# Optimization experiments

Measured on AMD Instinct MI355X. Metric: run time of the kernel, lower is better.

The kernel has to match this reference:

```python
import jax, jax.numpy as jnp
import numpy as np

B, S, D = 4, 2048, 1024
H = 16
HD = D // H


def setup_inputs() -> dict:
    key = jax.random.key(0)
    ks = jax.random.split(key, 5)
    scale = 0.02
    return {
        "x": jax.random.normal(ks[0], (B, S, D), dtype=jnp.float32),
        "wq": jax.random.normal(ks[1], (D, D), dtype=jnp.float32) * scale,
        "wk": jax.random.normal(ks[2], (D, D), dtype=jnp.float32) * scale,
        "wv": jax.random.normal(ks[3], (D, D), dtype=jnp.float32) * scale,
        "wo": jax.random.normal(ks[4], (D, D), dtype=jnp.float32) * scale,
    }


def reference(x, wq, wk, wv, wo):
    b, s, _ = x.shape
    # project and split heads: [b, h, s, hd]
    def proj(w):
        return jnp.einsum('bsd,de->bse', x, w).reshape(b, s, H, HD).transpose(0, 2, 1, 3)
    q, k, v = proj(wq), proj(wk), proj(wv)
    scores = jnp.einsum('bhqd,bhkd->bhqk', q, k)
    causal = jnp.tril(jnp.ones((s, s), dtype=bool))  # True = keep
    scores = jnp.where(causal, scores, -jnp.inf)
    attn = jax.nn.softmax(scores / jnp.sqrt(jnp.float32(HD)), axis=-1)
    ctx = jnp.einsum('bhqk,bhkd->bhqd', attn, v)
    ctx = ctx.transpose(0, 2, 1, 3).reshape(b, s, D)
    return jnp.einsum('bsd,de->bse', ctx, wo)
```

## Files before the change

### kernel.cpp

```cpp
#include <hip/hip_runtime.h>

#define S_LEN 2048
#define D_DIM 1024
#define NH    16
#define HD    64
#define BATCH 4
#define M_ROWS 8192

typedef __attribute__((ext_vector_type(8))) short bf16x8;
typedef __attribute__((ext_vector_type(4))) float f32x4;
typedef __attribute__((ext_vector_type(16))) float f32x16;
typedef __attribute__((ext_vector_type(8))) unsigned short u16x8;

__device__ __forceinline__ unsigned short f2bf(float f) {
    unsigned u = __builtin_bit_cast(unsigned, f);
    u = (u + 0x7fffu + ((u >> 16) & 1u)) >> 16;
    return (unsigned short)u;
}

__device__ __forceinline__ void gload16(const void* g, void* l) {
    __builtin_amdgcn_global_load_lds((const __attribute__((address_space(1))) unsigned*)g,
                                     (__attribute__((address_space(3))) unsigned*)l,
                                     16, 0, 0);
}

template<int N> __device__ __forceinline__ void vmwait() {
    if constexpr (N == 0)      asm volatile("s_waitcnt vmcnt(0)" ::: "memory");
    else if constexpr (N == 3) asm volatile("s_waitcnt vmcnt(3)" ::: "memory");
    else if constexpr (N == 5) asm volatile("s_waitcnt vmcnt(5)" ::: "memory");
}

__device__ __forceinline__ unsigned cvtpk_bf16(float lo, float hi) {
    unsigned r;
    asm("v_cvt_pk_bf16_f32 %0, %1, %2" : "=v"(r) : "v"(lo), "v"(hi));
    return r;
}
__device__ __forceinline__ void pl32swap(unsigned &a, unsigned &b) {
    asm("v_permlane32_swap_b32 %0, %1" : "+v"(a), "+v"(b));
}

__global__ __launch_bounds__(256) void prep_k(const float* __restrict__ x,
                                              const float* __restrict__ w0, const float* __restrict__ w1,
                                              const float* __restrict__ w2, const float* __restrict__ w3,
                                              unsigned short* __restrict__ xbf,
                                              unsigned short* __restrict__ o0, unsigned short* __restrict__ o1,
                                              unsigned short* __restrict__ o2, unsigned short* __restrict__ o3) {
    __shared__ float sT[64][65];
    const int t = threadIdx.x;
    if (blockIdx.x < 4096) {
        size_t i = (size_t)blockIdx.x * 256 + t;
        const float4* xf = (const float4*)x;
        float4 a = xf[2 * i], b = xf[2 * i + 1];
        u16x8 v;
        v[0] = f2bf(a.x); v[1] = f2bf(a.y); v[2] = f2bf(a.z); v[3] = f2bf(a.w);
        v[4] = f2bf(b.x); v[5] = f2bf(b.y); v[6] = f2bf(b.z); v[7] = f2bf(b.w);
        *(u16x8*)(xbf + i * 8) = v;
        return;
    }
    const int wb = blockIdx.x - 4096;
    const int z = wb >> 8;
    const float* w; unsigned short* o;
    switch (z) {
        case 0: w = w0; o = o0; break;
        case 1: w = w1; o = o1; break;
        case 2: w = w2; o = o2; break;
        default: w = w3; o = o3; break;
    }
    const float sc = (z == 0) ? 0.18033688011112042f : 1.0f;
    const int n0 = (wb & 15) * 64, k0 = ((wb >> 4) & 15) * 64;
    const int r = t >> 4, cq = t & 15;
#pragma unroll
    for (int it = 0; it < 4; ++it) {
        int k = r + it * 16;
        float4 v = *(const float4*)&w[(size_t)(k0 + k) * D_DIM + n0 + cq * 4];
        sT[k][cq * 4 + 0] = v.x; sT[k][cq * 4 + 1] = v.y;
        sT[k][cq * 4 + 2] = v.z; sT[k][cq * 4 + 3] = v.w;
    }
    __syncthreads();
    const int n = t >> 2, ch = t & 3;
    union { unsigned short s[8]; uint4 v; } p0, p1;
#pragma unroll
    for (int j = 0; j < 8; ++j) p0.s[j] = f2bf(sT[ch * 16 + j][n] * sc);
#pragma unroll
    for (int j = 0; j < 8; ++j) p1.s[j] = f2bf(sT[ch * 16 + 8 + j][n] * sc);
    *(uint4*)&o[(size_t)(n0 + n) * D_DIM + k0 + ch * 16]     = p0.v;
    *(uint4*)&o[(size_t)(n0 + n) * D_DIM + k0 + ch * 16 + 8] = p1.v;
}

template<int MFRAG, int NFRAG, int AGLD, int BGLD>
__device__ __forceinline__ void gemm_core(const unsigned short* __restrict__ A,
                                          const unsigned short* __restrict__ Bt,
                                          unsigned short* __restrict__ sA,
                                          unsigned short* __restrict__ sB,
                                          int m0, int n0, int t,
                                          f32x4 (&acc)[MFRAG][NFRAG])
{
    constexpr int NGLD  = AGLD + BGLD;
    constexpr int ASLOT = AGLD * 4096;
    constexpr int BSLOT = BGLD * 4096;
    constexpr int NPH   = MFRAG / 2;

    const int lane = t & 63, wid = t >> 6;
    const int mm = lane & 15, quad = lane >> 4;
    const int wm = wid >> 2, wn = wid & 3;

    const int sr = t >> 2;
    const int sg = (t & 3) ^ ((sr >> 1) & 3);
    const unsigned short* asrc = A  + (size_t)(m0 + sr) * D_DIM + sg * 8;
    const unsigned short* bsrc = Bt + (size_t)(n0 + sr) * D_DIM + sg * 8;
    unsigned short* dA = sA + t * 8;
    unsigned short* dB = sB + t * 8;

    const int al = wm * (MFRAG * 16) + mm;
    const int bl = wn * (NFRAG * 16) + mm;
    const int xs = quad ^ ((mm >> 1) & 3);

#pragma unroll
    for (int pt = 0; pt < 2; ++pt) {
        const int ko = pt * 32;
#pragma unroll
        for (int i = 0; i < AGLD; ++i)
            gload16(asrc + (size_t)i * 128 * D_DIM + ko, dA + pt * ASLOT + i * 4096);
#pragma unroll
        for (int i = 0; i < BGLD; ++i)
            gload16(bsrc + (size_t)i * 128 * D_DIM + ko, dB + pt * BSLOT + i * 4096);
    }
    vmwait<NGLD>();
    __builtin_amdgcn_s_barrier();

    int sRead = 0, sWrite = 2;
    for (int T = 0; T < 32; ++T) {
        const int soA = sRead * ASLOT, soB = sRead * BSLOT;
        const int woA = sWrite * ASLOT, woB = sWrite * BSLOT;
        const int ko = (T + 2) * 32;
        const bool st = (T <= 29);

        bf16x8 bv[NFRAG];
#pragma unroll
        for (int p = 0; p < NPH; ++p) {
            if (p == 0) {
#pragma unroll
                for (int nf = 0; nf < NFRAG; ++nf)
                    bv[nf] = *(const bf16x8*)&sB[soB + (bl + nf * 16) * 32 + xs * 8];
            }
            bf16x8 af0 = *(const bf16x8*)&sA[soA + (al + (2 * p) * 16) * 32 + xs * 8];
            bf16x8 af1 = *(const bf16x8*)&sA[soA + (al + (2 * p + 1) * 16) * 32 + xs * 8];

            if (st) {
                if (p == 0) {
#pragma unroll
                    for (int i = 0; i < AGLD; ++i)
                        gload16(asrc + (size_t)i * 128 * D_DIM + ko, dA + woA + i * 4096);
                } else {
#pragma unroll
                    for (int i = 0; i < BGLD; ++i)
                        if ((i % (NPH - 1)) == p - 1)
                            gload16(bsrc + (size_t)i * 128 * D_DIM + ko, dB + woB + i * 4096);
                }
            }

            __builtin_amdgcn_s_barrier();
            asm volatile("s_waitcnt lgkmcnt(0)" ::: "memory");
            __builtin_amdgcn_s_setprio(1);
#pragma unroll
            for (int nf = 0; nf < NFRAG; ++nf) {
                acc[2 * p][nf]     = __builtin_amdgcn_mfma_f32_16x16x32_bf16(af0, bv[nf], acc[2 * p][nf], 0, 0, 0);
                acc[2 * p + 1][nf] = __builtin_amdgcn_mfma_f32_16x16x32_bf16(af1, bv[nf], acc[2 * p + 1][nf], 0, 0, 0);
            }
            __builtin_amdgcn_s_setprio(0);
            if (p == NPH - 1) {
                if (T <= 29)      vmwait<NGLD>();
                else if (T == 30) vmwait<0>();
            }
            __builtin_amdgcn_s_barrier();
        }

        sRead  = (sRead  == 2) ? 0 : sRead + 1;
        sWrite = (sWrite == 2) ? 0 : sWrite + 1;
    }
}

__global__ __launch_bounds__(512, 2) void gemmqkv_k(const unsigned short* __restrict__ A,
                                                    const unsigned short* __restrict__ Bt,
                                                    unsigned short* __restrict__ qb,
                                                    unsigned short* __restrict__ kb,
                                                    unsigned short* __restrict__ vt)
{
    __shared__ unsigned short sA[3 * 2 * 4096];
    __shared__ unsigned short sB[3 * 3 * 4096];
    const int t = threadIdx.x;
    const int bid = blockIdx.x;
    const int wg = (bid & 7) * 32 + (bid >> 3);
    const int mt = wg >> 3, nt = wg & 7;
    const int m0 = mt * 256, n0 = nt * 384;

    f32x4 acc[8][6];
#pragma unroll
    for (int i = 0; i < 8; ++i)
#pragma unroll
        for (int j = 0; j < 6; ++j) acc[i][j] = (f32x4){0.f, 0.f, 0.f, 0.f};

    gemm_core<8, 6, 2, 3>(A, Bt, sA, sB, m0, n0, t, acc);

    const int lane = t & 63, wid = t >> 6;
    const int mm = lane & 15, quad = lane >> 4;
    const int wm = wid >> 2, wn = wid & 3;

#pragma unroll
    for (int nf = 0; nf < 6; ++nf) {
        const int c0 = n0 + wn * 96 + nf * 16;
        const int widx = c0 >> 10, nl0 = c0 & 1023;
        if (widx == 2) {
            const int h = nl0 >> 6, hd = (nl0 & 63) + mm;
#pragma unroll
            for (int mf = 0; mf < 8; ++mf) {
                int rglob = m0 + wm * 128 + mf * 16 + quad * 4;
                int bb = rglob >> 11, ss = rglob & (S_LEN - 1);
                union { unsigned short s[4]; unsigned long long ll; } pk;
#pragma unroll
                for (int r = 0; r < 4; ++r) pk.s[r] = f2bf(acc[mf][nf][r]);
                *(unsigned long long*)&vt[((size_t)(bb * NH + h) * HD + hd) * S_LEN + ss] = pk.ll;
            }
        } else {
            unsigned short* outp = widx ? kb : qb;
#pragma unroll
            for (int mf = 0; mf < 8; ++mf)
#pragma unroll
                for (int r = 0; r < 4; ++r)
                    outp[(size_t)(m0 + wm * 128 + mf * 16 + quad * 4 + r) * D_DIM +
                         nl0 + mm] = f2bf(acc[mf][nf][r]);
        }
    }
}

__global__ __launch_bounds__(512, 2) void gemmo_k(const unsigned short* __restrict__ A,
                                                  const unsigned short* __restrict__ Bt,
                                                  float* __restrict__ C)
{
    __shared__ unsigned short sA[3 * 4096];
    __shared__ unsigned short sB[3 * 2 * 4096];
    const int t = threadIdx.x;
    const int bid = blockIdx.x;
    const int wg = (bid & 7) * 32 + (bid >> 3);
    const int mt = wg >> 2, nt = wg & 3;
    const int m0 = mt * 128, n0 = nt * 256;

    f32x4 acc[4][4];
#pragma unroll
    for (int i = 0; i < 4; ++i)
#pragma unroll
        for (int j = 0; j < 4; ++j) acc[i][j] = (f32x4){0.f, 0.f, 0.f, 0.f};

    gemm_core<4, 4, 1, 2>(A, Bt, sA, sB, m0, n0, t, acc);

    const int lane = t & 63, wid = t >> 6;
    const int mm = lane & 15, quad = lane >> 4;
    const int wm = wid >> 2, wn = wid & 3;

#pragma unroll
    for (int mf = 0; mf < 4; ++mf)
#pragma unroll
        for (int nf = 0; nf < 4; ++nf)
#pragma unroll
            for (int r = 0; r < 4; ++r)
                C[(size_t)(m0 + wm * 64 + mf * 16 + quad * 4 + r) * D_DIM +
                  n0 + wn * 64 + nf * 16 + mm] = acc[mf][nf][r];
}

__global__ __launch_bounds__(256, 4) void attn_k(const unsigned short* __restrict__ Q,
                                                 const unsigned short* __restrict__ K,
                                                 const unsigned short* __restrict__ Vt,
                                                 unsigned short* __restrict__ ctx)
{
    __shared__ unsigned short sK [2][64 * 64];
    __shared__ unsigned short sVT[2][64 * 64];
    const int t = threadIdx.x;
    const int lane = t & 63, w = t >> 6;
    const int m5 = lane & 31, h = lane >> 5;
    const int m7 = m5 & 7;
    const int bid = blockIdx.x;
    const int c = bid & 255, j = bid >> 8;
    const int xcd = c & 7, u = (c >> 3) & 3, bhl = c >> 5;
    const int bh = xcd * 8 + bhl;
    const int qt = 4 * j + ((j & 1) ? (3 - u) : u);
    const int b = bh >> 4, hh = bh & 15;
    const size_t rowbase = (size_t)b * S_LEN;
    const int coff = hh * HD;
    const unsigned short* Vh = Vt + (size_t)bh * HD * S_LEN;

    const int sc = t >> 3, sj = t & 7;
    const int sg = (sj ^ (sc & 7)) * 8;

    u16x8 onesu;
#pragma unroll
    for (int jj = 0; jj < 8; ++jj) onesu[jj] = 0x3F80;
    const bf16x8 ones = __builtin_bit_cast(bf16x8, onesu);

    const int q0 = qt * 128;
    const int qrw = q0 + w * 32;
    const int qr  = qrw + m5;

    bf16x8 qf[4];
#pragma unroll
    for (int s = 0; s < 4; ++s)
        qf[s] = *(const bf16x8*)(Q + (rowbase + qr) * D_DIM + coff + s * 16 + h * 8);

    f32x16 o0, o1, l16;
#pragma unroll
    for (int r = 0; r < 16; ++r) { o0[r] = 0.f; o1[r] = 0.f; l16[r] = 0.f; }

    const int nkt = 2 * qt + 2;

    gload16(K  + (rowbase + sc) * D_DIM + coff + sg,      (void*)&sK[0][t * 8]);
    gload16(K  + (rowbase + sc + 32) * D_DIM + coff + sg, (void*)&sK[0][2048 + t * 8]);
    gload16(Vh + (size_t)sc * S_LEN + sg,                 (void*)&sVT[0][t * 8]);
    gload16(Vh + (size_t)(sc + 32) * S_LEN + sg,          (void*)&sVT[0][2048 + t * 8]);

    for (int kt = 0; kt < nkt; ++kt) {
        const int buf = kt & 1;
        __syncthreads();
        if (kt + 1 < nkt) {
            const int k1 = (kt + 1) * 64;
            gload16(K  + (rowbase + k1 + sc) * D_DIM + coff + sg,      (void*)&sK[1 - buf][t * 8]);
            gload16(K  + (rowbase + k1 + sc + 32) * D_DIM + coff + sg, (void*)&sK[1 - buf][2048 + t * 8]);
            gload16(Vh + (size_t)sc * S_LEN + k1 + sg,                 (void*)&sVT[1 - buf][t * 8]);
            gload16(Vh + (size_t)(sc + 32) * S_LEN + k1 + sg,          (void*)&sVT[1 - buf][2048 + t * 8]);
        }
        const int k0 = kt * 64;
        if (k0 > qrw + 31) continue;

        f32x16 s0, s1;
#pragma unroll
        for (int r = 0; r < 16; ++r) { s0[r] = 0.f; s1[r] = 0.f; }
        __builtin_amdgcn_s_setprio(1);
#pragma unroll
        for (int s = 0; s < 4; ++s) {
            const int sl = ((2 * s + h) ^ m7) * 8;
            bf16x8 ak0 = *(const bf16x8*)&sK[buf][m5 * 64 + sl];
            bf16x8 ak1 = *(const bf16x8*)&sK[buf][(32 + m5) * 64 + sl];
            s0 = __builtin_amdgcn_mfma_f32_32x32x16_bf16(ak0, qf[s], s0, 0, 0, 0);
            s1 = __builtin_amdgcn_mfma_f32_32x32x16_bf16(ak1, qf[s], s1, 0, 0, 0);
        }
        __builtin_amdgcn_s_setprio(0);

        const bool needmask = (k0 + 63) > qrw;
        bf16x8 pb[4];
#pragma unroll
        for (int kf = 0; kf < 2; ++kf) {
            unsigned pw[8];
#pragma unroll
            for (int jj = 0; jj < 8; ++jj) {
                float plo = __builtin_amdgcn_exp2f(kf ? s1[2 * jj] : s0[2 * jj]);
                float phi = __builtin_amdgcn_exp2f(kf ? s1[2 * jj + 1] : s0[2 * jj + 1]);
                if (needmask) {
                    const int kb_ = k0 + kf * 32 + 4 * h;
                    const int r0 = 2 * jj, r1 = 2 * jj + 1;
                    if (kb_ + (r0 & 3) + 8 * (r0 >> 2) > qr) plo = 0.f;
                    if (kb_ + (r1 & 3) + 8 * (r1 >> 2) > qr) phi = 0.f;
                }
                pw[jj] = cvtpk_bf16(plo, phi);
            }
            pl32swap(pw[0], pw[2]);
            pl32swap(pw[1], pw[3]);
            pl32swap(pw[4], pw[6]);
            pl32swap(pw[5], pw[7]);
            union { unsigned u4[4]; bf16x8 v; } f0, f1;
            f0.u4[0] = pw[0]; f0.u4[1] = pw[1]; f0.u4[2] = pw[2]; f0.u4[3] = pw[3];
            f1.u4[0] = pw[4]; f1.u4[1] = pw[5]; f1.u4[2] = pw[6]; f1.u4[3] = pw[7];
            pb[kf * 2 + 0] = f0.v;
            pb[kf * 2 + 1] = f1.v;
        }

        __builtin_amdgcn_s_setprio(1);
#pragma unroll
        for (int s = 0; s < 4; ++s) {
            const int sl = ((2 * s + h) ^ m7) * 8;
            bf16x8 vf0 = *(const bf16x8*)&sVT[buf][m5 * 64 + sl];
            bf16x8 vf1 = *(const bf16x8*)&sVT[buf][(32 + m5) * 64 + sl];
            l16 = __builtin_amdgcn_mfma_f32_32x32x16_bf16(ones, pb[s], l16, 0, 0, 0);
            o0  = __builtin_amdgcn_mfma_f32_32x32x16_bf16(vf0,  pb[s], o0, 0, 0, 0);
            o1  = __builtin_amdgcn_mfma_f32_32x32x16_bf16(vf1,  pb[s], o1, 0, 0, 0);
        }
        __builtin_amdgcn_s_setprio(0);
    }

    const float linv = 1.f / l16[0];
#pragma unroll
    for (int hf = 0; hf < 2; ++hf) {
#pragma unroll
        for (int rg = 0; rg < 4; ++rg) {
            union { unsigned short s4[4]; unsigned long long ll; } pk4;
#pragma unroll
            for (int r = 0; r < 4; ++r)
                pk4.s4[r] = f2bf((hf ? o1[rg * 4 + r] : o0[rg * 4 + r]) * linv);
            *(unsigned long long*)&ctx[(rowbase + qr) * D_DIM + coff + hf * 32 + 8 * rg + 4 * h] = pk4.ll;
        }
    }
}

extern "C" void kernel_launch(void* const* d_in, const int* in_sizes, int n_in,
                              void* d_out, int out_size, void* d_ws, size_t ws_size,
                              hipStream_t stream)
{
    const float* x  = (const float*)d_in[0];
    const float* wq = (const float*)d_in[1];
    const float* wk = (const float*)d_in[2];
    const float* wv = (const float*)d_in[3];
    const float* wo = (const float*)d_in[4];

    const size_t XE = (size_t)M_ROWS * D_DIM;
    const size_t WE = (size_t)D_DIM * D_DIM;
    unsigned short* ws  = (unsigned short*)d_ws;
    unsigned short* xbf = ws;
    unsigned short* wt0 = xbf + XE;
    unsigned short* wt1 = wt0 + WE;
    unsigned short* wt2 = wt1 + WE;
    unsigned short* wt3 = wt2 + WE;
    unsigned short* qb  = wt3 + WE;
    unsigned short* kb  = qb + XE;
    unsigned short* vt  = kb + XE;
    unsigned short* cb  = vt + XE;

    prep_k<<<dim3(4096 + 1024), 256, 0, stream>>>(x, wq, wk, wv, wo,
                                                  xbf, wt0, wt1, wt2, wt3);

    gemmqkv_k<<<dim3(256), 512, 0, stream>>>(xbf, wt0, qb, kb, vt);

    attn_k<<<dim3(1024), 256, 0, stream>>>(qb, kb, vt, cb);

    gemmo_k<<<dim3(256), 512, 0, stream>>>(cb, wt3, (float*)d_out);
}
```

Measured before the change: 238.4 us.

## Split causal attention KV ranges into balanced halves with separate combine kernel

Each attention block now processes two half-workloads: strip a's first KV range and strip (15-a)'s second KV range, so every block does roughly equal causal work. Unnormalized partial outputs and row sums are written in fp32 to a workspace, and a new combine kernel sums the two partials per strip, normalizes, and converts to bf16 ctx. This targets the load imbalance of the causal triangle across blocks. In exchange it adds about 64 MB of fp32 partial traffic and an extra kernel launch, and it relies on the workspace being large enough.

```diff
diff --git a/kernel.cpp b/kernel.cpp
--- a/kernel.cpp
+++ b/kernel.cpp
@@ -270,7 +270,8 @@
 __global__ __launch_bounds__(256, 4) void attn_k(const unsigned short* __restrict__ Q,
                                                  const unsigned short* __restrict__ K,
                                                  const unsigned short* __restrict__ Vt,
-                                                 unsigned short* __restrict__ ctx)
+                                                 float* __restrict__ PO,
+                                                 float* __restrict__ PL)
 {
     __shared__ unsigned short sK [2][64 * 64];
     __shared__ unsigned short sVT[2][64 * 64];
@@ -279,10 +280,8 @@
     const int m5 = lane & 31, h = lane >> 5;
     const int m7 = m5 & 7;
     const int bid = blockIdx.x;
-    const int c = bid & 255, j = bid >> 8;
-    const int xcd = c & 7, u = (c >> 3) & 3, bhl = c >> 5;
+    const int xcd = bid & 7, bhl = (bid >> 3) & 7, a = bid >> 6;
     const int bh = xcd * 8 + bhl;
-    const int qt = 4 * j + ((j & 1) ? (3 - u) : u);
     const int b = bh >> 4, hh = bh & 15;
     const size_t rowbase = (size_t)b * S_LEN;
     const int coff = hh * HD;
@@ -296,105 +295,145 @@
     for (int jj = 0; jj < 8; ++jj) onesu[jj] = 0x3F80;
     const bf16x8 ones = __builtin_bit_cast(bf16x8, onesu);
 
-    const int q0 = qt * 128;
-    const int qrw = q0 + w * 32;
-    const int qr  = qrw + m5;
-
-    bf16x8 qf[4];
-#pragma unroll
-    for (int s = 0; s < 4; ++s)
-        qf[s] = *(const bf16x8*)(Q + (rowbase + qr) * D_DIM + coff + s * 16 + h * 8);
-
-    f32x16 o0, o1, l16;
-#pragma unroll
-    for (int r = 0; r < 16; ++r) { o0[r] = 0.f; o1[r] = 0.f; l16[r] = 0.f; }
-
-    const int nkt = 2 * qt + 2;
-
-    gload16(K  + (rowbase + sc) * D_DIM + coff + sg,      (void*)&sK[0][t * 8]);
-    gload16(K  + (rowbase + sc + 32) * D_DIM + coff + sg, (void*)&sK[0][2048 + t * 8]);
-    gload16(Vh + (size_t)sc * S_LEN + sg,                 (void*)&sVT[0][t * 8]);
-    gload16(Vh + (size_t)(sc + 32) * S_LEN + sg,          (void*)&sVT[0][2048 + t * 8]);
-
-    for (int kt = 0; kt < nkt; ++kt) {
-        const int buf = kt & 1;
+#pragma unroll 1
+    for (int jidx = 0; jidx < 2; ++jidx) {
+        const int strip = jidx ? (15 - a) : a;
+        const int ktlo  = jidx ? (strip + 1) : 0;
+        const int kthi  = jidx ? (2 * strip + 1) : strip;
+
+        const int q0 = strip * 128;
+        const int qrw = q0 + w * 32;
+        const int qr  = qrw + m5;
+
+        bf16x8 qf[4];
+#pragma unroll
+        for (int s = 0; s < 4; ++s)
+            qf[s] = *(const bf16x8*)(Q + (rowbase + qr) * D_DIM + coff + s * 16 + h * 8);
+
+        f32x16 o0, o1, l16;
+#pragma unroll
+        for (int r = 0; r < 16; ++r) { o0[r] = 0.f; o1[r] = 0.f; l16[r] = 0.f; }
+
+        {
+            const int k1 = ktlo * 64;
+            gload16(K  + (rowbase + k1 + sc) * D_DIM + coff + sg,      (void*)&sK[0][t * 8]);
+            gload16(K  + (rowbase + k1 + sc + 32) * D_DIM + coff + sg, (void*)&sK[0][2048 + t * 8]);
+            gload16(Vh + (size_t)sc * S_LEN + k1 + sg,                 (void*)&sVT[0][t * 8]);
+            gload16(Vh + (size_t)(sc + 32) * S_LEN + k1 + sg,          (void*)&sVT[0][2048 + t * 8]);
+        }
+
+        for (int kt = ktlo; kt <= kthi; ++kt) {
+            const int buf = (kt - ktlo) & 1;
+            __syncthreads();
+            if (kt < kthi) {
+                const int k1 = (kt + 1) * 64;
+                gload16(K  + (rowbase + k1 + sc) * D_DIM + coff + sg,      (void*)&sK[1 - buf][t * 8]);
+                gload16(K  + (rowbase + k1 + sc + 32) * D_DIM + coff + sg, (void*)&sK[1 - buf][2048 + t * 8]);
+                gload16(Vh + (size_t)sc * S_LEN + k1 + sg,                 (void*)&sVT[1 - buf][t * 8]);
+                gload16(Vh + (size_t)(sc + 32) * S_LEN + k1 + sg,          (void*)&sVT[1 - buf][2048 + t * 8]);
+            }
+            const int k0 = kt * 64;
+            if (k0 > qrw + 31) continue;
+
+            f32x16 s0, s1;
+#pragma unroll
+            for (int r = 0; r < 16; ++r) { s0[r] = 0.f; s1[r] = 0.f; }
+            __builtin_amdgcn_s_setprio(1);
+#pragma unroll
+            for (int s = 0; s < 4; ++s) {
+                const int sl = ((2 * s + h) ^ m7) * 8;
+                bf16x8 ak0 = *(const bf16x8*)&sK[buf][m5 * 64 + sl];
+                bf16x8 ak1 = *(const bf16x8*)&sK[buf][(32 + m5) * 64 + sl];
+                s0 = __builtin_amdgcn_mfma_f32_32x32x16_bf16(ak0, qf[s], s0, 0, 0, 0);
+                s1 = __builtin_amdgcn_mfma_f32_32x32x16_bf16(ak1, qf[s], s1, 0, 0, 0);
+            }
+            __builtin_amdgcn_s_setprio(0);
+
+            const bool needmask = (k0 + 63) > qrw;
+            bf16x8 pb[4];
+#pragma unroll
+            for (int kf = 0; kf < 2; ++kf) {
+                unsigned pw[8];
+#pragma unroll
+                for (int jj = 0; jj < 8; ++jj) {
+                    float plo = __builtin_amdgcn_exp2f(kf ? s1[2 * jj] : s0[2 * jj]);
+                    float phi = __builtin_amdgcn_exp2f(kf ? s1[2 * jj + 1] : s0[2 * jj + 1]);
+                    if (needmask) {
+                        const int kb_ = k0 + kf * 32 + 4 * h;
+                        const int r0 = 2 * jj, r1 = 2 * jj + 1;
+                        if (kb_ + (r0 & 3) + 8 * (r0 >> 2) > qr) plo = 0.f;
+                        if (kb_ + (r1 & 3) + 8 * (r1 >> 2) > qr) phi = 0.f;
+                    }
+                    pw[jj] = cvtpk_bf16(plo, phi);
+                }
+                pl32swap(pw[0], pw[2]);
+                pl32swap(pw[1], pw[3]);
+                pl32swap(pw[4], pw[6]);
+                pl32swap(pw[5], pw[7]);
+                union { unsigned u4[4]; bf16x8 v; } f0, f1;
+                f0.u4[0] = pw[0]; f0.u4[1] = pw[1]; f0.u4[2] = pw[2]; f0.u4[3] = pw[3];
+                f1.u4[0] = pw[4]; f1.u4[1] = pw[5]; f1.u4[2] = pw[6]; f1.u4[3] = pw[7];
+                pb[kf * 2 + 0] = f0.v;
+                pb[kf * 2 + 1] = f1.v;
+            }
+
+            __builtin_amdgcn_s_setprio(1);
+#pragma unroll
+            for (int s = 0; s < 4; ++s) {
+                const int sl = ((2 * s + h) ^ m7) * 8;
+                bf16x8 vf0 = *(const bf16x8*)&sVT[buf][m5 * 64 + sl];
+                bf16x8 vf1 = *(const bf16x8*)&sVT[buf][(32 + m5) * 64 + sl];
+                l16 = __builtin_amdgcn_mfma_f32_32x32x16_bf16(ones, pb[s], l16, 0, 0, 0);
+                o0  = __builtin_amdgcn_mfma_f32_32x32x16_bf16(vf0,  pb[s], o0, 0, 0, 0);
+                o1  = __builtin_amdgcn_mfma_f32_32x32x16_bf16(vf1,  pb[s], o1, 0, 0, 0);
+            }
+            __builtin_amdgcn_s_setprio(0);
+        }
         __syncthreads();
-        if (kt + 1 < nkt) {
-            const int k1 = (kt + 1) * 64;
-            gload16(K  + (rowbase + k1 + sc) * D_DIM + coff + sg,      (void*)&sK[1 - buf][t * 8]);
-            gload16(K  + (rowbase + k1 + sc + 32) * D_DIM + coff + sg, (void*)&sK[1 - buf][2048 + t * 8]);
-            gload16(Vh + (size_t)sc * S_LEN + k1 + sg,                 (void*)&sVT[1 - buf][t * 8]);
-            gload16(Vh + (size_t)(sc + 32) * S_LEN + k1 + sg,          (void*)&sVT[1 - buf][2048 + t * 8]);
+
+        const int jid = ((bh << 4) + strip) * 2 + jidx;
+        float* po = PO + (size_t)jid * 8192;
+        const int ql = w * 32 + m5;
+#pragma unroll
+        for (int hf = 0; hf < 2; ++hf) {
+#pragma unroll
+            for (int rg = 0; rg < 4; ++rg) {
+                f32x4 v;
+#pragma unroll
+                for (int r = 0; r < 4; ++r) v[r] = hf ? o1[rg * 4 + r] : o0[rg * 4 + r];
+                *(f32x4*)&po[ql * 64 + hf * 32 + 8 * rg + 4 * h] = v;
+            }
         }
-        const int k0 = kt * 64;
-        if (k0 > qrw + 31) continue;
-
-        f32x16 s0, s1;
-#pragma unroll
-        for (int r = 0; r < 16; ++r) { s0[r] = 0.f; s1[r] = 0.f; }
-        __builtin_amdgcn_s_setprio(1);
-#pragma unroll
-        for (int s = 0; s < 4; ++s) {
-            const int sl = ((2 * s + h) ^ m7) * 8;
-            bf16x8 ak0 = *(const bf16x8*)&sK[buf][m5 * 64 + sl];
-            bf16x8 ak1 = *(const bf16x8*)&sK[buf][(32 + m5) * 64 + sl];
-            s0 = __builtin_amdgcn_mfma_f32_32x32x16_bf16(ak0, qf[s], s0, 0, 0, 0);
-            s1 = __builtin_amdgcn_mfma_f32_32x32x16_bf16(ak1, qf[s], s1, 0, 0, 0);
-        }
-        __builtin_amdgcn_s_setprio(0);
-
-        const bool needmask = (k0 + 63) > qrw;
-        bf16x8 pb[4];
-#pragma unroll
-        for (int kf = 0; kf < 2; ++kf) {
-            unsigned pw[8];
-#pragma unroll
-            for (int jj = 0; jj < 8; ++jj) {
-                float plo = __builtin_amdgcn_exp2f(kf ? s1[2 * jj] : s0[2 * jj]);
-                float phi = __builtin_amdgcn_exp2f(kf ? s1[2 * jj + 1] : s0[2 * jj + 1]);
-                if (needmask) {
-                    const int kb_ = k0 + kf * 32 + 4 * h;
-                    const int r0 = 2 * jj, r1 = 2 * jj + 1;
-                    if (kb_ + (r0 & 3) + 8 * (r0 >> 2) > qr) plo = 0.f;
-                    if (kb_ + (r1 & 3) + 8 * (r1 >> 2) > qr) phi = 0.f;
-                }
-                pw[jj] = cvtpk_bf16(plo, phi);
-            }
-            pl32swap(pw[0], pw[2]);
-            pl32swap(pw[1], pw[3]);
-            pl32swap(pw[4], pw[6]);
-            pl32swap(pw[5], pw[7]);
-            union { unsigned u4[4]; bf16x8 v; } f0, f1;
-            f0.u4[0] = pw[0]; f0.u4[1] = pw[1]; f0.u4[2] = pw[2]; f0.u4[3] = pw[3];
-            f1.u4[0] = pw[4]; f1.u4[1] = pw[5]; f1.u4[2] = pw[6]; f1.u4[3] = pw[7];
-            pb[kf * 2 + 0] = f0.v;
-            pb[kf * 2 + 1] = f1.v;
-        }
-
-        __builtin_amdgcn_s_setprio(1);
-#pragma unroll
-        for (int s = 0; s < 4; ++s) {
-            const int sl = ((2 * s + h) ^ m7) * 8;
-            bf16x8 vf0 = *(const bf16x8*)&sVT[buf][m5 * 64 + sl];
-            bf16x8 vf1 = *(const bf16x8*)&sVT[buf][(32 + m5) * 64 + sl];
-            l16 = __builtin_amdgcn_mfma_f32_32x32x16_bf16(ones, pb[s], l16, 0, 0, 0);
-            o0  = __builtin_amdgcn_mfma_f32_32x32x16_bf16(vf0,  pb[s], o0, 0, 0, 0);
-            o1  = __builtin_amdgcn_mfma_f32_32x32x16_bf16(vf1,  pb[s], o1, 0, 0, 0);
-        }
-        __builtin_amdgcn_s_setprio(0);
-    }
-
-    const float linv = 1.f / l16[0];
-#pragma unroll
-    for (int hf = 0; hf < 2; ++hf) {
-#pragma unroll
-        for (int rg = 0; rg < 4; ++rg) {
-            union { unsigned short s4[4]; unsigned long long ll; } pk4;
-#pragma unroll
-            for (int r = 0; r < 4; ++r)
-                pk4.s4[r] = f2bf((hf ? o1[rg * 4 + r] : o0[rg * 4 + r]) * linv);
-            *(unsigned long long*)&ctx[(rowbase + qr) * D_DIM + coff + hf * 32 + 8 * rg + 4 * h] = pk4.ll;
-        }
+        if (h == 0) PL[(size_t)jid * 128 + ql] = l16[0];
+    }
+}
+
+__global__ __launch_bounds__(256) void combine_k(const float* __restrict__ PO,
+                                                 const float* __restrict__ PL,
+                                                 unsigned short* __restrict__ ctx)
+{
+    const int s = blockIdx.x;
+    const int bh = s >> 4, strip = s & 15;
+    const int b = bh >> 4, hh = bh & 15;
+    const size_t rowbase = (size_t)b * S_LEN + strip * 128;
+    const int coff = hh * HD;
+    const float* p0 = PO + (size_t)s * 16384;
+    const float* p1 = p0 + 8192;
+    const float* l0 = PL + (size_t)s * 256;
+    const float* l1 = l0 + 128;
+    const int t = threadIdx.x;
+
+#pragma unroll
+    for (int k = 0; k < 8; ++k) {
+        const int e = k * 1024 + t * 4;
+        const int q = e >> 6, hd = e & 63;
+        f32x4 va = *(const f32x4*)&p0[e];
+        f32x4 vb = *(const f32x4*)&p1[e];
+        const float inv = 1.f / (l0[q] + l1[q]);
+        union { unsigned short s4[4]; unsigned long long ll; } pk;
+#pragma unroll
+        for (int r = 0; r < 4; ++r) pk.s4[r] = f2bf((va[r] + vb[r]) * inv);
+        *(unsigned long long*)&ctx[(rowbase + q) * D_DIM + coff + hd] = pk.ll;
     }
 }
 
@@ -420,13 +459,17 @@
     unsigned short* kb  = qb + XE;
     unsigned short* vt  = kb + XE;
     unsigned short* cb  = vt + XE;
+    float* po = (float*)(cb + XE);
+    float* pl = po + (size_t)2048 * 8192;
 
     prep_k<<<dim3(4096 + 1024), 256, 0, stream>>>(x, wq, wk, wv, wo,
                                                   xbf, wt0, wt1, wt2, wt3);
 
     gemmqkv_k<<<dim3(256), 512, 0, stream>>>(xbf, wt0, qb, kb, vt);
 
-    attn_k<<<dim3(1024), 256, 0, stream>>>(qb, kb, vt, cb);
+    attn_k<<<dim3(1024), 256, 0, stream>>>(qb, kb, vt, po, pl);
+
+    combine_k<<<dim3(1024), 256, 0, stream>>>(po, pl, cb);
 
     gemmo_k<<<dim3(256), 512, 0, stream>>>(cb, wt3, (float*)d_out);
 }
```

Measured after the change: 251.3 us. 5.4% more time.
